# Optimization experiments

Hardware: AMD Instinct MI355X
Metric: run time of the kernel (lower is better)

## Reference

```python
import jax, jax.numpy as jnp
import numpy as np

N_G, E_G = 50000, 800000
N_S, E_S = 10000, 160000
NF = 64
B = 8

def _w(key, shape):
    fan_in = shape[-1]
    return jax.random.normal(key, shape, dtype=jnp.float32) / np.sqrt(fan_in)

def setup_inputs() -> dict:
    key = jax.random.key(0)
    ks = jax.random.split(key, 40)
    inp = {
        "graph_x": jax.random.normal(ks[0], (N_G, NF), dtype=jnp.float32),
        "subgraph_x": jax.random.normal(ks[1], (N_S, NF), dtype=jnp.float32),
        "point": jax.random.normal(ks[2], (B, NF), dtype=jnp.float32),
        "graph_edge_index": jax.random.randint(ks[3], (2, E_G), 0, N_G),
        "graph_batch": jnp.sort(jax.random.randint(ks[4], (N_G,), 0, B)),
        "subgraph_edge_index": jax.random.randint(ks[5], (2, E_S), 0, N_S),
        "subgraph_batch": jnp.sort(jax.random.randint(ks[6], (N_S,), 0, B)),
    }
    # GraphConv params per branch: channel sizes 64->128->256->192
    dims = [(2 * NF, NF), (4 * NF, 2 * NF), (3 * NF, 4 * NF)]
    i = 7
    for pre in ("g", "s"):
        for li, (o, c) in enumerate(dims, start=1):
            inp[f"{pre}W{li}r"] = _w(ks[i], (o, c)); i += 1  # lin_rel (aggregated)
            inp[f"{pre}W{li}n"] = _w(ks[i], (o, c)); i += 1  # lin_root (self)
            inp[f"{pre}B{li}"] = jnp.zeros((o,), dtype=jnp.float32)
    inp["l1W"] = _w(ks[i], (600, 3 * NF + 3 * NF + NF)); i += 1
    inp["l1b"] = jnp.zeros((600,), dtype=jnp.float32)
    inp["l2W"] = _w(ks[i], (256, 600)); i += 1
    inp["l2b"] = jnp.zeros((256,), dtype=jnp.float32)
    inp["l3W"] = _w(ks[i], (NF, 256)); i += 1
    inp["l3b"] = jnp.zeros((NF,), dtype=jnp.float32)
    return inp

def _graph_conv(x, src, dst, Wr, Wn, b, n_nodes):
    # PyG GraphConv: out_i = Wr @ sum_{j->i} x_j + Wn @ x_i + b
    agg = jax.ops.segment_sum(x[src], dst, num_segments=n_nodes)
    return agg @ Wr.T + x @ Wn.T + b

def _scatter_mean(x, seg, num_segments):
    s = jax.ops.segment_sum(x, seg, num_segments=num_segments)
    cnt = jax.ops.segment_sum(jnp.ones((x.shape[0],), x.dtype), seg, num_segments=num_segments)
    return s / jnp.maximum(cnt, 1.0)[:, None]

def _branch(x, edge_index, batch, params, n_nodes):
    src, dst = edge_index[0], edge_index[1]
    for (Wr, Wn, b) in params:
        x = jax.nn.elu(_graph_conv(x, src, dst, Wr, Wn, b, n_nodes))
    return _scatter_mean(x, batch, B)

def reference(graph_x, subgraph_x, point,
              gW1r, gW1n, gB1, gW2r, gW2n, gB2, gW3r, gW3n, gB3,
              sW1r, sW1n, sB1, sW2r, sW2n, sB2, sW3r, sW3n, sB3,
              l1W, l1b, l2W, l2b, l3W, l3b,
              graph_edge_index, graph_batch, subgraph_edge_index, subgraph_batch):
    x1 = _branch(graph_x, graph_edge_index, graph_batch,
                 [(gW1r, gW1n, gB1), (gW2r, gW2n, gB2), (gW3r, gW3n, gB3)], N_G)
    x2 = _branch(subgraph_x, subgraph_edge_index, subgraph_batch,
                 [(sW1r, sW1n, sB1), (sW2r, sW2n, sB2), (sW3r, sW3n, sB3)], N_S)
    x = jnp.concatenate([x1, x2, point], axis=-1)  # [B, 448]
    x = jax.nn.relu(x @ l1W.T + l1b)
    x = jax.nn.relu(x @ l2W.T + l2b)
    return x @ l3W.T + l3b  # [B, 64]
```

## Files before the change

kernel.cpp:

```cpp
#include <hip/hip_runtime.h>
#include <cmath>

typedef __attribute__((ext_vector_type(8))) short short8;
typedef __attribute__((ext_vector_type(4))) float floatx4;
typedef __attribute__((ext_vector_type(2))) float floatx2;
typedef __attribute__((ext_vector_type(4))) int intx4;
typedef __attribute__((ext_vector_type(2))) int intx2;

#define N_G 50000
#define E_G 800000
#define N_S 10000
#define E_S 160000
#define NT (N_G + N_S)
#define ET (E_G + E_S)
#define BATCH 8
#define STRIDE 64
#define FPASS 8

__device__ __forceinline__ short f2b(float f) {
    unsigned u = __builtin_bit_cast(unsigned, f);
    u += 0x7FFF + ((u >> 16) & 1);
    return (short)(u >> 16);
}
__device__ __forceinline__ short8 fp8x8_to_bf16(intx2 w) {
    floatx2 f0 = __builtin_amdgcn_cvt_pk_f32_fp8(w[0], false);
    floatx2 f1 = __builtin_amdgcn_cvt_pk_f32_fp8(w[0], true);
    floatx2 f2 = __builtin_amdgcn_cvt_pk_f32_fp8(w[1], false);
    floatx2 f3 = __builtin_amdgcn_cvt_pk_f32_fp8(w[1], true);
    short8 r;
    r[0]=f2b(f0[0]); r[1]=f2b(f0[1]); r[2]=f2b(f1[0]); r[3]=f2b(f1[1]);
    r[4]=f2b(f2[0]); r[5]=f2b(f2[1]); r[6]=f2b(f3[0]); r[7]=f2b(f3[1]);
    return r;
}
__device__ __forceinline__ void acc16(float* acc, intx4 w) {
    #pragma unroll
    for (int q = 0; q < 4; ++q) {
        floatx2 f0 = __builtin_amdgcn_cvt_pk_f32_fp8(w[q], false);
        floatx2 f1 = __builtin_amdgcn_cvt_pk_f32_fp8(w[q], true);
        acc[q * 4 + 0] += f0[0];
        acc[q * 4 + 1] += f0[1];
        acc[q * 4 + 2] += f1[0];
        acc[q * 4 + 3] += f1[1];
    }
}
__device__ __forceinline__ void gload_lds16(const void* g, void* l) {
    __builtin_amdgcn_global_load_lds(
        (const __attribute__((address_space(1))) unsigned int*)g,
        (__attribute__((address_space(3))) unsigned int*)l, 16, 0, 0);
}

struct RepArgs { const float* Wr[6]; const float* Wn[6]; short* dst[6]; int cin[6]; int nk[6]; int groups[6]; };
__global__ void init_kernel(const float* __restrict__ gx, const float* __restrict__ sx,
                            unsigned char* __restrict__ X0_8,
                            unsigned char* __restrict__ h1_8, unsigned char* __restrict__ h2_8,
                            int* __restrict__ dcount, float* __restrict__ pooled,
                            const int* __restrict__ g_batch, const int* __restrict__ s_batch,
                            int* __restrict__ starts, int* __restrict__ csr,
                            RepArgs ra, int total_groups) {
    int t = blockIdx.x * blockDim.x + threadIdx.x;
    if (t < NT * 16) {
        size_t e = (size_t)t * 4;
        const float* src = (e < (size_t)N_G * 64) ? (gx + e) : (sx + (e - (size_t)N_G * 64));
        floatx4 v = *(const floatx4*)src;
        int w8 = 0;
        w8 = __builtin_amdgcn_cvt_pk_fp8_f32(v[0], v[1], w8, false);
        w8 = __builtin_amdgcn_cvt_pk_fp8_f32(v[2], v[3], w8, true);
        *(unsigned int*)(X0_8 + e) = (unsigned int)w8;
        intx4 s4 = {NT, NT, NT, NT};
        *(intx4*)(csr + (size_t)t * 4) = s4;
    }
    if (t < NT) dcount[t] = 0;
    if (t < 16 * 192) pooled[t] = 0.f;
    if (t < 28) {
        intx4 z = {0, 0, 0, 0};
        if (t < 4)       *(intx4*)(X0_8 + (size_t)NT * 64  + t * 16) = z;
        else if (t < 12) *(intx4*)(h1_8 + (size_t)NT * 128 + (t - 4) * 16) = z;
        else             *(intx4*)(h2_8 + (size_t)NT * 256 + (t - 12) * 16) = z;
    }
    if (t <= 16) {
        int b = t;
        if (b == 16) { starts[16] = NT; }
        else {
            int key, n, base;
            const int* arr;
            if (b < 8) { arr = g_batch; n = N_G; key = b; base = 0; }
            else       { arr = s_batch; n = N_S; key = b - 8; base = N_G; }
            int lo = 0, hi = n;
            while (lo < hi) { int mid = (lo + hi) >> 1; if (arr[mid] < key) lo = mid + 1; else hi = mid; }
            starts[b] = base + lo;
        }
    }
    if (t < total_groups) {
        int seg = 0, off = t;
        while (seg < 5 && off >= ra.groups[seg]) { off -= ra.groups[seg]; ++seg; }
        int CIN = ra.cin[seg], NK = ra.nk[seg];
        int lane = off & 63;
        int rest = off >> 6;
        int tt = rest % NK;
        int ot = rest / NK;
        int o = ot * 16 + (lane & 15);
        int kk = tt * 32 + (lane >> 4) * 8;
        const float* src = (kk < CIN) ? (ra.Wr[seg] + (size_t)o * CIN + kk)
                                      : (ra.Wn[seg] + (size_t)o * CIN + (kk - CIN));
        floatx4 u0 = *(const floatx4*)src;
        floatx4 u1 = *(const floatx4*)(src + 4);
        short8 d;
        d[0]=f2b(u0[0]); d[1]=f2b(u0[1]); d[2]=f2b(u0[2]); d[3]=f2b(u0[3]);
        d[4]=f2b(u1[0]); d[5]=f2b(u1[1]); d[6]=f2b(u1[2]); d[7]=f2b(u1[3]);
        *(short8*)(ra.dst[seg] + (size_t)off * 8) = d;
    }
}

__global__ void fill_kernel(const int* __restrict__ g_ei, const int* __restrict__ s_ei,
                            int* __restrict__ dcount, int* __restrict__ csr) {
    int pass = blockIdx.x & (FPASS - 1);
    int lb   = blockIdx.x >> 3;
    int t = lb * blockDim.x + threadIdx.x;
    if (t >= ET) return;
    int dst;
    if (t < E_G) dst = g_ei[E_G + t];
    else         dst = s_ei[E_S + (t - E_G)] + N_G;
    int lo = pass * (NT / FPASS);
    int hi = lo + (NT / FPASS);
    if (dst < lo || dst >= hi) return;
    int src;
    if (t < E_G) src = g_ei[t];
    else         src = s_ei[t - E_G] + N_G;
    int slot = atomicAdd(&dcount[dst], 1);
    if (slot < STRIDE) csr[(size_t)dst * STRIDE + slot] = src;
}

template<int C>
__global__ __launch_bounds__(256) void agg8_kernel(const unsigned char* __restrict__ x8,
                            const int* __restrict__ dcount,
                            const int* __restrict__ csr, short* __restrict__ out) {
    constexpr int C16 = C / 16;
    int t = blockIdx.x * blockDim.x + threadIdx.x;
    if (t >= NT * C16) return;
    int node = t / C16;
    int ch   = t % C16;
    const int* crow = csr + (size_t)node * STRIDE;
    int deg8 = (min(dcount[node], STRIDE) + 7) & ~7;
    const unsigned char* xb = x8 + (size_t)ch * 16;
    float acc[16];
    #pragma unroll
    for (int j = 0; j < 16; ++j) acc[j] = 0.f;
    for (int e = 0; e < deg8; e += 8) {
        intx4 i0 = *(const intx4*)(crow + e);
        intx4 i1 = *(const intx4*)(crow + e + 4);
        intx4 w0 = *(const intx4*)(xb + (size_t)i0[0] * C);
        intx4 w1 = *(const intx4*)(xb + (size_t)i0[1] * C);
        intx4 w2 = *(const intx4*)(xb + (size_t)i0[2] * C);
        intx4 w3 = *(const intx4*)(xb + (size_t)i0[3] * C);
        intx4 w4 = *(const intx4*)(xb + (size_t)i1[0] * C);
        intx4 w5 = *(const intx4*)(xb + (size_t)i1[1] * C);
        intx4 w6 = *(const intx4*)(xb + (size_t)i1[2] * C);
        intx4 w7 = *(const intx4*)(xb + (size_t)i1[3] * C);
        acc16(acc, w0); acc16(acc, w1); acc16(acc, w2); acc16(acc, w3);
        acc16(acc, w4); acc16(acc, w5); acc16(acc, w6); acc16(acc, w7);
    }
    short8 o0, o1;
    #pragma unroll
    for (int j = 0; j < 8; ++j) { o0[j] = f2b(acc[j]); o1[j] = f2b(acc[8 + j]); }
    short8* q = (short8*)(out + (size_t)node * C + ch * 16);
    q[0] = o0; q[1] = o1;
}

template<int CIN, int COUT, bool POOL>
__global__ __launch_bounds__(256) void gemm_elu_kernel(
        const short* __restrict__ A1, const unsigned char* __restrict__ A2_8,
        const short* __restrict__ gWF, const short* __restrict__ sWF,
        const float* __restrict__ gB, const float* __restrict__ sB,
        unsigned char* __restrict__ out8,
        float* __restrict__ pooled, const int* __restrict__ starts) {
    constexpr int NK  = CIN / 16;
    constexpr int NOT = COUT / 16;
    constexpr int TILE_SH = NK * 512;
    constexpr int MAX_SH = 16384;
    constexpr int CHUNK_OT = (NOT * TILE_SH <= MAX_SH) ? NOT : (MAX_SH / TILE_SH);
    static_assert(NOT % CHUNK_OT == 0, "chunk must divide NOT");
    constexpr int CH_SH = CHUNK_OT * TILE_SH;
    __shared__ short lds[CH_SH];

    int wave = threadIdx.x >> 6;
    int lane = threadIdx.x & 63;
    int tile0 = blockIdx.x << 2;
    int myTile = tile0 + wave;
    bool active = myTile < (NT / 16);
    int tileC = active ? myTile : (NT / 16 - 1);
    int r0 = tileC * 16;
    bool sub = (r0 >= N_G);
    const short* WF = sub ? sWF : gWF;
    const float* bias = sub ? sB : gB;
    int id = lane & 15, quad = lane >> 4;
    int arow = r0 + id;
    short8 a[NK];
    #pragma unroll
    for (int t = 0; t < NK; ++t) {
        int kk = t * 32 + quad * 8;
        if (kk < CIN) {
            a[t] = *(const short8*)(A1 + (size_t)arow * CIN + kk);
        } else {
            intx2 w = *(const intx2*)(A2_8 + (size_t)arow * CIN + (kk - CIN));
            a[t] = fp8x8_to_bf16(w);
        }
    }
    int seg0 = 0, seg1 = 0;
    if (POOL) {
        while (seg0 < 15 && starts[seg0 + 1] <= r0) ++seg0;
        seg1 = seg0;
        while (seg1 < 15 && starts[seg1 + 1] <= r0 + 15) ++seg1;
    }

    constexpr int BTILE = N_G / 16;
    int lastTile = min(tile0 + 3, NT / 16 - 1);
    bool mixed = (tile0 < BTILE) && (lastTile >= BTILE);

    auto epilogue = [&](int ot, floatx4 acc) {
        int o = ot * 16 + id;
        float bv = bias[o];
        float vr[4];
        #pragma unroll
        for (int r = 0; r < 4; ++r) {
            float v = acc[r] + bv;
            vr[r] = (v > 0.f) ? v : (expf(v) - 1.f);
        }
        if (!active) return;
        if (!POOL) {
            #pragma unroll
            for (int r = 0; r < 4; ++r) {
                int nrow = r0 + quad * 4 + r;
                int w8 = __builtin_amdgcn_cvt_pk_fp8_f32(vr[r], vr[r], 0, false);
                out8[(size_t)nrow * COUT + o] = (unsigned char)(w8 & 0xFF);
            }
        } else if (seg0 == seg1) {
            float vsum = vr[0] + vr[1] + vr[2] + vr[3];
            vsum += __shfl_down(vsum, 32, 64);
            vsum += __shfl_down(vsum, 16, 64);
            if (lane < 16) atomicAdd(&pooled[seg0 * 192 + o], vsum);
        } else {
            #pragma unroll
            for (int r = 0; r < 4; ++r) {
                int nrow = r0 + quad * 4 + r;
                int sg = seg0;
                while (sg < seg1 && starts[sg + 1] <= nrow) ++sg;
                atomicAdd(&pooled[sg * 192 + o], vr[r]);
            }
        }
    };

    if (!mixed) {
        for (int c0 = 0; c0 < NOT; c0 += CHUNK_OT) {
            const short* src = WF + (size_t)c0 * TILE_SH;
            #pragma unroll 4
            for (int i = threadIdx.x * 8; i < CH_SH; i += 256 * 8) {
                *(short8*)&lds[i] = *(const short8*)&src[i];
            }
            __syncthreads();
            #pragma unroll
            for (int otl = 0; otl < CHUNK_OT; ++otl) {
                floatx4 acc = {0.f, 0.f, 0.f, 0.f};
                const short* wp = &lds[otl * TILE_SH + lane * 8];
                #pragma unroll
                for (int t = 0; t < NK; ++t) {
                    short8 b = *(const short8*)(wp + t * 512);
                    acc = __builtin_amdgcn_mfma_f32_16x16x32_bf16(a[t], b, acc, 0, 0, 0);
                }
                epilogue(c0 + otl, acc);
            }
            __syncthreads();
        }
    } else {
        for (int ot = 0; ot < NOT; ++ot) {
            floatx4 acc = {0.f, 0.f, 0.f, 0.f};
            const short* wp = WF + (((size_t)ot * NK) * 64 + lane) * 8;
            #pragma unroll
            for (int t = 0; t < NK; ++t) {
                short8 b = *(const short8*)(wp + (size_t)t * 64 * 8);
                acc = __builtin_amdgcn_mfma_f32_16x16x32_bf16(a[t], b, acc, 0, 0, 0);
            }
            epilogue(ot, acc);
        }
    }
}

__global__ __launch_bounds__(256) void mlp1_kernel(
        const float* __restrict__ pooled, const int* __restrict__ starts,
        const float* __restrict__ point, const float* __restrict__ W,
        const float* __restrict__ bias, float* __restrict__ out) {
    int wave = (blockIdx.x * blockDim.x + threadIdx.x) >> 6;
    int lane = threadIdx.x & 63;
    if (wave >= BATCH * 600) return;
    int b = wave / 600, o = wave % 600;
    float invg = 1.f / (float)max(starts[b + 1] - starts[b], 1);
    float invs = 1.f / (float)max(starts[9 + b] - starts[8 + b], 1);
    const float* w = W + (size_t)o * 448;
    float acc = 0.f;
    for (int i = lane; i < 448; i += 64) {
        float x;
        if (i < 192)      x = pooled[b * 192 + i] * invg;
        else if (i < 384) x = pooled[(8 + b) * 192 + (i - 192)] * invs;
        else              x = point[b * 64 + (i - 384)];
        acc += x * w[i];
    }
    #pragma unroll
    for (int off = 32; off > 0; off >>= 1) acc += __shfl_down(acc, off, 64);
    if (lane == 0) out[wave] = fmaxf(acc + bias[o], 0.f);
}

__global__ __launch_bounds__(256) void dense_wave_kernel(
        const float* __restrict__ in, const float* __restrict__ W,
        const float* __restrict__ bias, float* __restrict__ out,
        int I, int O, int relu) {
    int wave = (blockIdx.x * blockDim.x + threadIdx.x) >> 6;
    int lane = threadIdx.x & 63;
    if (wave >= BATCH * O) return;
    int b = wave / O, o = wave % O;
    const float* x = in + (size_t)b * I;
    const float* w = W + (size_t)o * I;
    float acc = 0.f;
    for (int i = lane; i < I; i += 64) acc += x[i] * w[i];
    #pragma unroll
    for (int off = 32; off > 0; off >>= 1) acc += __shfl_down(acc, off, 64);
    if (lane == 0) {
        acc += bias[o];
        if (relu) acc = fmaxf(acc, 0.f);
        out[wave] = acc;
    }
}

extern "C" void kernel_launch(void* const* d_in, const int* in_sizes, int n_in,
                              void* d_out, int out_size, void* d_ws, size_t ws_size,
                              hipStream_t stream) {
    const float* graph_x = (const float*)d_in[0];
    const float* sub_x   = (const float*)d_in[1];
    const float* point   = (const float*)d_in[2];
    const int*   g_ei    = (const int*)d_in[3];
    const int*   g_batch = (const int*)d_in[4];
    const int*   s_ei    = (const int*)d_in[5];
    const int*   s_batch = (const int*)d_in[6];
    const float* gB1=(const float*)d_in[9],  *gB2=(const float*)d_in[12], *gB3=(const float*)d_in[15];
    const float* sB1=(const float*)d_in[18], *sB2=(const float*)d_in[21], *sB3=(const float*)d_in[24];
    const float* l1W=(const float*)d_in[25], *l1b=(const float*)d_in[26];
    const float* l2W=(const float*)d_in[27], *l2b=(const float*)d_in[28];
    const float* l3W=(const float*)d_in[29], *l3b=(const float*)d_in[30];

    char* ws = (char*)d_ws;
    size_t off = 0;
    auto alloc = [&](size_t bytes) -> char* {
        char* p = ws + off;
        off = (off + bytes + 255) & ~(size_t)255;
        return p;
    };
    int* dcount = (int*)alloc((size_t)NT * 4);
    int* csr = (int*)alloc((size_t)NT * STRIDE * 4);

    const int fsz[3] = {128 * 2 * 64, 256 * 2 * 128, 192 * 2 * 256};
    short* wfrag = (short*)alloc((size_t)(fsz[0] + fsz[1] + fsz[2]) * 2 * 2);
    short* gWF[3], *sWF[3];
    { size_t o2 = 0;
      for (int l = 0; l < 3; ++l) { gWF[l] = wfrag + o2; o2 += fsz[l]; }
      for (int l = 0; l < 3; ++l) { sWF[l] = wfrag + o2; o2 += fsz[l]; } }

    unsigned char* X0_8 = (unsigned char*)alloc((size_t)(NT + 1) * 64);
    short* agg = (short*)alloc((size_t)NT * 256 * 2);
    unsigned char* h1_8 = (unsigned char*)alloc((size_t)(NT + 1) * 128);
    unsigned char* h2_8 = (unsigned char*)alloc((size_t)(NT + 1) * 256);

    float* pooled = (float*)alloc(16 * 192 * 4);
    int* starts = (int*)alloc(17 * 4);
    float* mlp_h1 = (float*)alloc(BATCH * 600 * 4);
    float* mlp_h2 = (float*)alloc(BATCH * 256 * 4);

    RepArgs ra;
    const int cin_l[3] = {64, 128, 256};
    const int nk_l[3]  = {4, 8, 16};
    const int not_l[3] = {8, 16, 12};
    const int wr_idx[6] = {7, 10, 13, 16, 19, 22};
    int total_groups = 0;
    for (int s = 0; s < 6; ++s) {
        int l = s % 3;
        ra.Wr[s] = (const float*)d_in[wr_idx[s]];
        ra.Wn[s] = (const float*)d_in[wr_idx[s] + 1];
        ra.dst[s] = (s < 3) ? gWF[l] : sWF[l];
        ra.cin[s] = cin_l[l];
        ra.nk[s] = nk_l[l];
        ra.groups[s] = not_l[l] * nk_l[l] * 64;
        total_groups += ra.groups[s];
    }

    init_kernel<<<(NT * 16 + 255) / 256, 256, 0, stream>>>(graph_x, sub_x, X0_8, h1_8, h2_8,
                                                           dcount, pooled, g_batch, s_batch,
                                                           starts, csr, ra, total_groups);

    fill_kernel<<<((ET + 255) / 256) * FPASS, 256, 0, stream>>>(g_ei, s_ei, dcount, csr);

    constexpr int NW = NT / 16;
    const int gemm_blocks = (NW + 3) / 4;

    agg8_kernel<64><<<(NT * 4 + 255) / 256, 256, 0, stream>>>(X0_8, dcount, csr, agg);
    gemm_elu_kernel<64, 128, false><<<gemm_blocks, 256, 0, stream>>>(
        agg, X0_8, gWF[0], sWF[0], gB1, sB1, h1_8, nullptr, nullptr);
    agg8_kernel<128><<<(NT * 8 + 255) / 256, 256, 0, stream>>>(h1_8, dcount, csr, agg);
    gemm_elu_kernel<128, 256, false><<<gemm_blocks, 256, 0, stream>>>(
        agg, h1_8, gWF[1], sWF[1], gB2, sB2, h2_8, nullptr, nullptr);
    agg8_kernel<256><<<(NT * 16 + 255) / 256, 256, 0, stream>>>(h2_8, dcount, csr, agg);
    gemm_elu_kernel<256, 192, true><<<gemm_blocks, 256, 0, stream>>>(
        agg, h2_8, gWF[2], sWF[2], gB3, sB3, nullptr, pooled, starts);

    mlp1_kernel<<<(BATCH * 600 + 3) / 4, 256, 0, stream>>>(pooled, starts, point, l1W, l1b, mlp_h1);
    dense_wave_kernel<<<(BATCH * 256 + 3) / 4, 256, 0, stream>>>(mlp_h1, l2W, l2b, mlp_h2, 600, 256, 1);
    dense_wave_kernel<<<(BATCH * 64 + 3) / 4, 256, 0, stream>>>(mlp_h2, l3W, l3b, (float*)d_out, 256, 64, 0);
}
```

Baseline: 345.8 us.

## Double-buffer weight chunks in LDS with direct global-to-LDS loads

The GEMM+ELU kernel now stages weight tiles into two fixed 8192-element LDS buffers using direct global-to-LDS loads. The next chunk is prefetched while MFMAs run on the current one, so weight loading overlaps compute instead of being followed by a barrier stall. The ELU also switches from expf to the faster __expf intrinsic. In exchange, chunks are smaller for small layers, which means more barriers. Correctness also relies on the async loads being complete before each barrier, and the exponential is slightly less accurate.

```diff
diff --git a/kernel.cpp b/kernel.cpp
--- a/kernel.cpp
+++ b/kernel.cpp
@@ -176,11 +176,12 @@
     constexpr int NK  = CIN / 16;
     constexpr int NOT = COUT / 16;
     constexpr int TILE_SH = NK * 512;
-    constexpr int MAX_SH = 16384;
-    constexpr int CHUNK_OT = (NOT * TILE_SH <= MAX_SH) ? NOT : (MAX_SH / TILE_SH);
+    constexpr int CHUNK_SH = 8192;
+    constexpr int CHUNK_OT = CHUNK_SH / TILE_SH;
     static_assert(NOT % CHUNK_OT == 0, "chunk must divide NOT");
-    constexpr int CH_SH = CHUNK_OT * TILE_SH;
-    __shared__ short lds[CH_SH];
+    constexpr int NC = NOT / CHUNK_OT;
+    constexpr int SREG = CHUNK_SH / 2048;
+    __shared__ short lds[2][CHUNK_SH];
 
     int wave = threadIdx.x >> 6;
     int lane = threadIdx.x & 63;
@@ -223,7 +224,7 @@
         #pragma unroll
         for (int r = 0; r < 4; ++r) {
             float v = acc[r] + bv;
-            vr[r] = (v > 0.f) ? v : (expf(v) - 1.f);
+            vr[r] = (v > 0.f) ? v : (__expf(v) - 1.f);
         }
         if (!active) return;
         if (!POOL) {
@@ -250,23 +251,27 @@
     };
 
     if (!mixed) {
-        for (int c0 = 0; c0 < NOT; c0 += CHUNK_OT) {
-            const short* src = WF + (size_t)c0 * TILE_SH;
-            #pragma unroll 4
-            for (int i = threadIdx.x * 8; i < CH_SH; i += 256 * 8) {
-                *(short8*)&lds[i] = *(const short8*)&src[i];
-            }
-            __syncthreads();
+        auto stage = [&](int c, int buf) {
+            const short* src = WF + (size_t)c * CHUNK_SH + threadIdx.x * 8;
+            short* dst = &lds[buf][threadIdx.x * 8];
+            #pragma unroll
+            for (int i = 0; i < SREG; ++i)
+                gload_lds16(src + i * 2048, dst + i * 2048);
+        };
+        stage(0, 0);
+        __syncthreads();
+        for (int c = 0; c < NC; ++c) {
+            if (c + 1 < NC) stage(c + 1, (c + 1) & 1);
+            const short* base = &lds[c & 1][lane * 8];
             #pragma unroll
             for (int otl = 0; otl < CHUNK_OT; ++otl) {
                 floatx4 acc = {0.f, 0.f, 0.f, 0.f};
-                const short* wp = &lds[otl * TILE_SH + lane * 8];
                 #pragma unroll
                 for (int t = 0; t < NK; ++t) {
-                    short8 b = *(const short8*)(wp + t * 512);
+                    short8 b = *(const short8*)(base + otl * TILE_SH + t * 512);
                     acc = __builtin_amdgcn_mfma_f32_16x16x32_bf16(a[t], b, acc, 0, 0, 0);
                 }
-                epilogue(c0 + otl, acc);
+                epilogue(c * CHUNK_OT + otl, acc);
             }
             __syncthreads();
         }
```

Result: no change. 345.1 us (-0.2%).
